# Optimization experiments

Measured on AMD Instinct MI355X. Metric: run time of the kernel, lower is better.

## Reference

```python
import jax, jax.numpy as jnp
import numpy as np

N_IN, N_HIDDEN = 64, 1024
N, K = 8192, 16


def _linear_params(key, fan_in, fan_out):
    k1, k2 = jax.random.split(key)
    bound = 1.0 / np.sqrt(fan_in)
    W = jax.random.uniform(k1, (fan_in, fan_out), minval=-bound, maxval=bound, dtype=jnp.float32)
    b = jax.random.uniform(k2, (fan_out,), minval=-bound, maxval=bound, dtype=jnp.float32)
    return W, b


def setup_inputs() -> dict:
    key = jax.random.key(0)
    keys = jax.random.split(key, 7)
    towers = jax.random.normal(keys[0], (N, K, N_IN), dtype=jnp.float32)
    aggregate = jnp.zeros((1, N_HIDDEN), dtype=jnp.float32)
    MW1, Mb1 = _linear_params(keys[1], N_IN + N_HIDDEN, N_HIDDEN)
    MW2, Mb2 = _linear_params(keys[2], N_HIDDEN, N_HIDDEN)
    MW3, Mb3 = _linear_params(keys[3], N_HIDDEN, N_HIDDEN)
    OW1, Ob1 = _linear_params(keys[4], N_IN + N_HIDDEN, N_HIDDEN)
    OW2, Ob2 = _linear_params(keys[5], N_HIDDEN, N_HIDDEN)
    OW3, Ob3 = _linear_params(keys[6], N_HIDDEN, 1)
    return {"towers": towers, "aggregate": aggregate,
            "MW1": MW1, "Mb1": Mb1, "MW2": MW2, "Mb2": Mb2, "MW3": MW3, "Mb3": Mb3,
            "OW1": OW1, "Ob1": Ob1, "OW2": OW2, "Ob2": Ob2, "OW3": OW3, "Ob3": Ob3}


def reference(towers, aggregate, MW1, Mb1, MW2, Mb2, MW3, Mb3, OW1, Ob1, OW2, Ob2, OW3, Ob3):
    N_, K_, _ = towers.shape
    summary0 = jnp.broadcast_to(aggregate, (N_, aggregate.shape[1]))

    def step(summary, tower_k):
        # tower_k: (N, n_in); summary: (N, n_hidden)
        x = jnp.concatenate([summary, tower_k], axis=1)  # (N, n_hidden + n_in)
        h = jax.nn.relu(x @ OW1 + Ob1)
        h = jax.nn.relu(h @ OW2 + Ob2)
        pred = jax.nn.sigmoid(h @ OW3 + Ob3)[:, 0]  # (N,)
        m = jax.nn.relu(x @ MW1 + Mb1)
        m = jax.nn.relu(m @ MW2 + Mb2)
        m = jax.nn.relu(m @ MW3 + Mb3)
        return m, pred

    towers_k_first = jnp.transpose(towers, (1, 0, 2))  # (K, N, n_in)
    _, preds = jax.lax.scan(step, summary0, towers_k_first)  # preds: (K, N)
    return jnp.prod(preds, axis=0)  # (N,)
```

## Files before the change

### kernel.cpp

```cpp
#include <hip/hip_runtime.h>
#include <cstdint>
#include <cstddef>


typedef _Float16 f16x8 __attribute__((ext_vector_type(8)));
typedef float f32x16 __attribute__((ext_vector_type(16)));

__device__ __forceinline__ void gload16(const void* g, void* l) {
  __builtin_amdgcn_global_load_lds(
      (__attribute__((address_space(1))) void*)const_cast<void*>(g),
      (__attribute__((address_space(3))) void*)l,
      16, 0, 0);
}

__global__ __launch_bounds__(256, 3)
void gemm_h_kernel(const _Float16* __restrict__ A0, int ldA0,
                   const _Float16* __restrict__ A1, int ldA1,
                   int kcut, int Ktot,
                   const _Float16* __restrict__ B,
                   const float* __restrict__ bias,
                   _Float16* __restrict__ C, int ldC,
                   const float* __restrict__ w3, float* __restrict__ sacc)
{
  __shared__ _Float16 sAh[128 * 64];
  __shared__ _Float16 sBh[128 * 64];

  const int lane = threadIdx.x & 63;
  const int wave = threadIdx.x >> 6;
  const int wm = (wave >> 1) * 64, wn = (wave & 1) * 64;
  const int mBase = blockIdx.x * 128, nBase = blockIdx.y * 128;

  const int lr = lane >> 3;
  const int lcs8 = ((lane & 7) ^ lr) * 8;

  const int l31 = lane & 31, l5 = lane >> 5;
  const int fswz = l31 & 7;

  f32x16 acc[2][2];
#pragma unroll
  for (int i = 0; i < 2; ++i)
#pragma unroll
    for (int j = 0; j < 2; ++j)
      acc[i][j] = (f32x16)0.0f;

  for (int kt = 0; kt < Ktot; kt += 64) {
    const _Float16* aH; int pA, kl;
    if (kt < kcut) { aH = A0; pA = ldA0; kl = kt; }
    else           { aH = A1; pA = ldA1; kl = kt - kcut; }

#pragma unroll
    for (int cc = 0; cc < 4; ++cc) {
      const int c = wave * 4 + cc;
      const int arow = mBase + c * 8 + lr;
      const int brow = nBase + c * 8 + lr;
      gload16(aH + (size_t)arow * pA   + kl + lcs8, &sAh[c * 512]);
      gload16(B  + (size_t)brow * Ktot + kt + lcs8, &sBh[c * 512]);
    }
    __syncthreads();

#pragma unroll
    for (int kh = 0; kh < 4; ++kh) {
      const int ko = ((kh * 2 + l5) ^ fswz) * 8;
      f16x8 ah[2], bh[2];
#pragma unroll
      for (int i = 0; i < 2; ++i)
        ah[i] = *(const f16x8*)&sAh[(wm + i * 32 + l31) * 64 + ko];
#pragma unroll
      for (int j = 0; j < 2; ++j)
        bh[j] = *(const f16x8*)&sBh[(wn + j * 32 + l31) * 64 + ko];
#pragma unroll
      for (int i = 0; i < 2; ++i)
#pragma unroll
        for (int j = 0; j < 2; ++j)
          acc[i][j] = __builtin_amdgcn_mfma_f32_32x32x16_f16(ah[i], bh[j], acc[i][j], 0, 0, 0);
    }
    __syncthreads();
  }

  float bv[2], w3v[2];
#pragma unroll
  for (int j = 0; j < 2; ++j) {
    const int col = nBase + wn + j * 32 + l31;
    bv[j] = bias[col];
    w3v[j] = sacc ? w3[col] : 0.0f;
  }

  if (sacc) {
#pragma unroll
    for (int i = 0; i < 2; ++i)
#pragma unroll
      for (int r = 0; r < 16; ++r) {
        float pr = 0.0f;
#pragma unroll
        for (int j = 0; j < 2; ++j)
          pr += fmaxf(acc[i][j][r] + bv[j], 0.0f) * w3v[j];
        pr += __shfl_xor(pr, 1);
        pr += __shfl_xor(pr, 2);
        pr += __shfl_xor(pr, 4);
        pr += __shfl_xor(pr, 8);
        pr += __shfl_xor(pr, 16);
        if (l31 == 0)
          atomicAdd(&sacc[mBase + wm + i * 32 + (r & 3) + 8 * (r >> 2) + 4 * l5], pr);
      }
  } else {
#pragma unroll
    for (int i = 0; i < 2; ++i)
#pragma unroll
      for (int j = 0; j < 2; ++j)
#pragma unroll
        for (int r = 0; r < 16; ++r) {
          const int row = mBase + wm + i * 32 + (r & 3) + 8 * (r >> 2) + 4 * l5;
          const int col = nBase + wn + j * 32 + l31;
          float v = fmaxf(acc[i][j][r] + bv[j], 0.0f);
          C[(size_t)row * ldC + col] = (_Float16)v;
        }
  }
}

__global__ void wconv_kernel(const float* __restrict__ W, int K, int N,
                             _Float16* __restrict__ oH) {
  int idx = blockIdx.x * 256 + threadIdx.x;
  if (idx >= K * N) return;
  int n = idx / K, k = idx - n * K;
  oH[idx] = (_Float16)W[(size_t)k * N + n];
}

__global__ void init_summary_kernel(const float* __restrict__ agg,
                                    _Float16* __restrict__ sH,
                                    float* __restrict__ sacc) {
  int idx = blockIdx.x * 256 + threadIdx.x;
  sH[idx] = (_Float16)agg[idx & 1023];
  if (idx < 8192) sacc[idx] = 0.0f;
}

__global__ void biascat_kernel(const float* __restrict__ b0,
                               const float* __restrict__ b1,
                               float* __restrict__ o) {
  int idx = blockIdx.x * 256 + threadIdx.x;
  o[idx] = (idx < 1024) ? b0[idx] : b1[idx - 1024];
}

__global__ void tow_conv_all_kernel(const float* __restrict__ towers,
                                    _Float16* __restrict__ oH) {
  size_t idx = (size_t)blockIdx.x * 256 + threadIdx.x;
  int f = idx & 63;
  int n = (int)((idx >> 6) & 8191);
  int k = (int)(idx >> 19);
  oH[idx] = (_Float16)towers[((size_t)n * 16 + k) * 64 + f];
}

__global__ void pred_final_kernel(float* __restrict__ sacc, const float* __restrict__ b3,
                                  float* __restrict__ out, int step) {
  int row = blockIdx.x * 256 + threadIdx.x;
  float p = 1.0f / (1.0f + expf(-(sacc[row] + b3[0])));
  out[row] = (step == 0) ? p : out[row] * p;
  sacc[row] = 0.0f;
}

extern "C" void kernel_launch(void* const* d_in, const int* in_sizes, int n_in,
                              void* d_out, int out_size, void* d_ws, size_t ws_size,
                              hipStream_t stream) {
  const float* towers = (const float*)d_in[0];
  const float* agg    = (const float*)d_in[1];
  const float* MW1 = (const float*)d_in[2];
  const float* Mb1 = (const float*)d_in[3];
  const float* MW2 = (const float*)d_in[4];
  const float* Mb2 = (const float*)d_in[5];
  const float* MW3 = (const float*)d_in[6];
  const float* Mb3 = (const float*)d_in[7];
  const float* OW1 = (const float*)d_in[8];
  const float* Ob1 = (const float*)d_in[9];
  const float* OW2 = (const float*)d_in[10];
  const float* Ob2 = (const float*)d_in[11];
  const float* OW3 = (const float*)d_in[12];
  const float* Ob3 = (const float*)d_in[13];
  float* out = (float*)d_out;

  _Float16* p = (_Float16*)d_ws;
  _Float16* W1catH = p; p += (size_t)2048 * 1088;
  _Float16* MW2tH  = p; p += (size_t)1024 * 1024;
  _Float16* OW2tH  = p; p += (size_t)1024 * 1024;
  _Float16* MW3tH  = p; p += (size_t)1024 * 1024;
  _Float16* sumH   = p; p += (size_t)8192 * 1024;
  _Float16* mh1    = p; p += (size_t)8192 * 2048;
  _Float16* m2H    = p; p += (size_t)8192 * 1024;
  _Float16* towAllH = p; p += (size_t)16 * 8192 * 64;
  float* sacc  = (float*)p;
  float* b1cat = sacc + 8192;

  {
    int tot = 1088 * 1024;
    wconv_kernel<<<dim3((tot + 255) / 256), dim3(256), 0, stream>>>(MW1, 1088, 1024, W1catH);
    wconv_kernel<<<dim3((tot + 255) / 256), dim3(256), 0, stream>>>(OW1, 1088, 1024, W1catH + (size_t)1024 * 1088);
    tot = 1024 * 1024;
    wconv_kernel<<<dim3((tot + 255) / 256), dim3(256), 0, stream>>>(MW2, 1024, 1024, MW2tH);
    wconv_kernel<<<dim3((tot + 255) / 256), dim3(256), 0, stream>>>(OW2, 1024, 1024, OW2tH);
    wconv_kernel<<<dim3((tot + 255) / 256), dim3(256), 0, stream>>>(MW3, 1024, 1024, MW3tH);
    biascat_kernel<<<dim3(8), dim3(256), 0, stream>>>(Mb1, Ob1, b1cat);
    init_summary_kernel<<<dim3(32768), dim3(256), 0, stream>>>(agg, sumH, sacc);
    tow_conv_all_kernel<<<dim3(32768), dim3(256), 0, stream>>>(towers, towAllH);
  }

  const dim3 G1(64, 16), G(64, 8), B256(256);
  for (int k = 0; k < 16; ++k) {
    const _Float16* towH = towAllH + (size_t)k * 8192 * 64;

    gemm_h_kernel<<<G1, B256, 0, stream>>>(sumH, 1024, towH, 64, 1024, 1088,
                                           W1catH, b1cat, mh1, 2048, nullptr, nullptr);
    gemm_h_kernel<<<G, B256, 0, stream>>>(mh1, 2048, mh1, 2048, 1024, 1024,
                                          MW2tH, Mb2, m2H, 1024, nullptr, nullptr);
    gemm_h_kernel<<<G, B256, 0, stream>>>(mh1 + 1024, 2048, mh1 + 1024, 2048, 1024, 1024,
                                          OW2tH, Ob2, nullptr, 1024, OW3, sacc);
    gemm_h_kernel<<<G, B256, 0, stream>>>(m2H, 1024, m2H, 1024, 1024, 1024,
                                          MW3tH, Mb3, sumH, 1024, nullptr, nullptr);
    pred_final_kernel<<<dim3(32), dim3(256), 0, stream>>>(sacc, Ob3, out, k);
  }
}
```

Measured before the change: 2.107 ms.

## Merge per-step GEMM launches into paired and pred-fused kernels

The two independent second-layer GEMMs (message and output towers) now run in a single launch using blockIdx.z to pick operands. The sigmoid/product prediction step is folded into the third message GEMM launch as an extra grid row. This cuts per-step launches from five to three and lets the two independent GEMMs share the device at once, at the cost of per-block branching and mixed work in one grid.

Result: faster. 2.007 ms (-4.7%).

```diff
diff --git a/kernel.cpp b/kernel.cpp
--- a/kernel.cpp
+++ b/kernel.cpp
@@ -13,14 +13,15 @@
       16, 0, 0);
 }
 
-__global__ __launch_bounds__(256, 3)
-void gemm_h_kernel(const _Float16* __restrict__ A0, int ldA0,
-                   const _Float16* __restrict__ A1, int ldA1,
-                   int kcut, int Ktot,
-                   const _Float16* __restrict__ B,
-                   const float* __restrict__ bias,
-                   _Float16* __restrict__ C, int ldC,
-                   const float* __restrict__ w3, float* __restrict__ sacc)
+__device__ __forceinline__ void gemm_core(
+    const _Float16* __restrict__ A0, int ldA0,
+    const _Float16* __restrict__ A1, int ldA1,
+    int kcut, int Ktot,
+    const _Float16* __restrict__ B,
+    const float* __restrict__ bias,
+    _Float16* __restrict__ C, int ldC,
+    const float* __restrict__ w3, float* __restrict__ sacc,
+    int mBase, int nBase)
 {
   __shared__ _Float16 sAh[128 * 64];
   __shared__ _Float16 sBh[128 * 64];
@@ -28,7 +29,6 @@
   const int lane = threadIdx.x & 63;
   const int wave = threadIdx.x >> 6;
   const int wm = (wave >> 1) * 64, wn = (wave & 1) * 64;
-  const int mBase = blockIdx.x * 128, nBase = blockIdx.y * 128;
 
   const int lr = lane >> 3;
   const int lcs8 = ((lane & 7) ^ lr) * 8;
@@ -117,6 +117,58 @@
   }
 }
 
+__global__ __launch_bounds__(256, 3)
+void gemm_h_kernel(const _Float16* __restrict__ A0, int ldA0,
+                   const _Float16* __restrict__ A1, int ldA1,
+                   int kcut, int Ktot,
+                   const _Float16* __restrict__ B,
+                   const float* __restrict__ bias,
+                   _Float16* __restrict__ C, int ldC,
+                   const float* __restrict__ w3, float* __restrict__ sacc)
+{
+  gemm_core(A0, ldA0, A1, ldA1, kcut, Ktot, B, bias, C, ldC, w3, sacc,
+            blockIdx.x * 128, blockIdx.y * 128);
+}
+
+__global__ __launch_bounds__(256, 3)
+void gemm_pair_kernel(const _Float16* __restrict__ Am,
+                      const _Float16* __restrict__ Ah, int ldA, int Ktot,
+                      const _Float16* __restrict__ Bm,
+                      const _Float16* __restrict__ Bh,
+                      const float* __restrict__ biasm,
+                      const float* __restrict__ biash,
+                      _Float16* __restrict__ Cm, int ldCm,
+                      const float* __restrict__ w3, float* __restrict__ sacc)
+{
+  const bool h = (blockIdx.z != 0);
+  gemm_core(h ? Ah : Am, ldA, h ? Ah : Am, ldA, Ktot, Ktot,
+            h ? Bh : Bm, h ? biash : biasm,
+            h ? nullptr : Cm, ldCm,
+            h ? w3 : nullptr, h ? sacc : nullptr,
+            blockIdx.x * 128, blockIdx.y * 128);
+}
+
+__global__ __launch_bounds__(256, 3)
+void gemm_pred_kernel(const _Float16* __restrict__ A, int ldA, int Ktot,
+                      const _Float16* __restrict__ B,
+                      const float* __restrict__ bias,
+                      _Float16* __restrict__ C, int ldC,
+                      float* __restrict__ sacc, const float* __restrict__ b3,
+                      float* __restrict__ out, int step)
+{
+  if (blockIdx.y == 8) {
+    if (blockIdx.x < 32) {
+      const int row = blockIdx.x * 256 + threadIdx.x;
+      float pv = 1.0f / (1.0f + expf(-(sacc[row] + b3[0])));
+      out[row] = (step == 0) ? pv : out[row] * pv;
+      sacc[row] = 0.0f;
+    }
+    return;
+  }
+  gemm_core(A, ldA, A, ldA, Ktot, Ktot, B, bias, C, ldC, nullptr, nullptr,
+            blockIdx.x * 128, blockIdx.y * 128);
+}
+
 __global__ void wconv_kernel(const float* __restrict__ W, int K, int N,
                              _Float16* __restrict__ oH) {
   int idx = blockIdx.x * 256 + threadIdx.x;
@@ -147,14 +199,6 @@
   int n = (int)((idx >> 6) & 8191);
   int k = (int)(idx >> 19);
   oH[idx] = (_Float16)towers[((size_t)n * 16 + k) * 64 + f];
-}
-
-__global__ void pred_final_kernel(float* __restrict__ sacc, const float* __restrict__ b3,
-                                  float* __restrict__ out, int step) {
-  int row = blockIdx.x * 256 + threadIdx.x;
-  float p = 1.0f / (1.0f + expf(-(sacc[row] + b3[0])));
-  out[row] = (step == 0) ? p : out[row] * p;
-  sacc[row] = 0.0f;
 }
 
 extern "C" void kernel_launch(void* const* d_in, const int* in_sizes, int n_in,
@@ -201,18 +245,16 @@
     tow_conv_all_kernel<<<dim3(32768), dim3(256), 0, stream>>>(towers, towAllH);
   }
 
-  const dim3 G1(64, 16), G(64, 8), B256(256);
+  const dim3 G1(64, 16), G2(64, 8, 2), G3(64, 9), B256(256);
   for (int k = 0; k < 16; ++k) {
     const _Float16* towH = towAllH + (size_t)k * 8192 * 64;
 
     gemm_h_kernel<<<G1, B256, 0, stream>>>(sumH, 1024, towH, 64, 1024, 1088,
                                            W1catH, b1cat, mh1, 2048, nullptr, nullptr);
-    gemm_h_kernel<<<G, B256, 0, stream>>>(mh1, 2048, mh1, 2048, 1024, 1024,
-                                          MW2tH, Mb2, m2H, 1024, nullptr, nullptr);
-    gemm_h_kernel<<<G, B256, 0, stream>>>(mh1 + 1024, 2048, mh1 + 1024, 2048, 1024, 1024,
-                                          OW2tH, Ob2, nullptr, 1024, OW3, sacc);
-    gemm_h_kernel<<<G, B256, 0, stream>>>(m2H, 1024, m2H, 1024, 1024, 1024,
-                                          MW3tH, Mb3, sumH, 1024, nullptr, nullptr);
-    pred_final_kernel<<<dim3(32), dim3(256), 0, stream>>>(sacc, Ob3, out, k);
-  }
-}
+    gemm_pair_kernel<<<G2, B256, 0, stream>>>(mh1, mh1 + 1024, 2048, 1024,
+                                              MW2tH, OW2tH, Mb2, Ob2,
+                                              m2H, 1024, OW3, sacc);
+    gemm_pred_kernel<<<G3, B256, 0, stream>>>(m2H, 1024, 1024, MW3tH, Mb3,
+                                              sumH, 1024, sacc, Ob3, out, k);
+  }
+}
```
